# Kernel tuning notes

Hardware: AMD Instinct MI355X
Metric: run time of the kernel (lower is better)

Reference implementation:

```python
import jax, jax.numpy as jnp
from jax import lax
import numpy as np

T, B, D, N = 1024, 32, 1024, 64
INIT_D_ALPHA, INIT_ALPHA_BIAS = 0.1, 2.0

def _xavier(key, n_out, n_in):
    lim = float(np.sqrt(6.0 / (n_in + n_out)))
    return jax.random.uniform(key, (n_out, n_in), jnp.float32, -lim, lim)

def setup_inputs() -> dict:
    key = jax.random.key(0)
    k = jax.random.split(key, 5)
    return {
        "x": jax.random.normal(k[0], (T, B, D), jnp.float32),
        "S0": jnp.zeros((B, N, N), jnp.float32),
        "W_k": _xavier(k[1], N, D),
        "W_v": _xavier(k[2], N, D),
        "W_q": _xavier(k[3], N, D),
        "W_alpha": _xavier(k[4], N, D),
        "d_alpha": jnp.full((N,), INIT_D_ALPHA, jnp.float32),
        "b_alpha": jnp.full((N,), INIT_ALPHA_BIAS, jnp.float32),
    }

def reference(x, S0, W_k, W_v, W_q, W_alpha, d_alpha, b_alpha):
    # Precompute all per-step projections as batched GEMMs: [T,B,N]
    k = jnp.einsum('tbd,nd->tbn', x, W_k)
    v = jnp.einsum('tbd,nd->tbn', x, W_v)
    q = jnp.einsum('tbd,nd->tbn', x, W_q)
    ax = jnp.einsum('tbd,nd->tbn', x, W_alpha)

    def step(S, inp):
        k_t, v_t, q_t, ax_t = inp  # each [B,N]
        retrieved = jnp.einsum('bij,bj->bi', S, k_t)            # S @ k
        alpha = jax.nn.sigmoid(ax_t + d_alpha * retrieved + b_alpha)  # [B,N]
        outer = v_t[:, :, None] * k_t[:, None, :]               # outer(v,k) [B,N,N]
        S = alpha[:, :, None] * S + (1.0 - alpha)[:, :, None] * outer
        h = jnp.einsum('bij,bj->bi', S, q_t)                    # S @ q
        out = h * jax.nn.silu(h)                                # self-gated
        return S, out

    S_final, output = lax.scan(step, S0, (k, v, q, ax))
    return output, S_final
```

## Files before the change

kernel.cpp:

```cpp
#include <hip/hip_runtime.h>
#include <math.h>

#define T_STEPS 1024
#define BATCH   32
#define DIM     1024
#define NST     64
#define TBN     ((size_t)T_STEPS * BATCH * NST)

typedef __attribute__((ext_vector_type(8))) short bf16x8;
typedef __attribute__((ext_vector_type(4))) float f32x4;

#define NLOG2E (-1.44269504088896340736f)

__device__ unsigned short g_khi[TBN];
__device__ unsigned short g_klo[TBN];
__device__ unsigned short g_qhi[TBN];
__device__ unsigned short g_qlo[TBN];


__device__ __forceinline__ void gload16(const float* g, float* l)
{
    __builtin_amdgcn_global_load_lds(
        (const __attribute__((address_space(1))) unsigned int*)g,
        (__attribute__((address_space(3))) unsigned int*)l, 16, 0, 0);
}

__device__ __forceinline__ void cvt8(float4 v0, float4 v1, bf16x8& hi, bf16x8& lo)
{
    float f[8] = {v0.x, v0.y, v0.z, v0.w, v1.x, v1.y, v1.z, v1.w};
    bf16x8 h, l;
    #pragma unroll
    for (int i = 0; i < 8; i++) {
        unsigned b = __float_as_uint(f[i]);
        h[i] = (short)(b >> 16);
        l[i] = (short)(__float_as_uint(f[i] - __uint_as_float(b & 0xffff0000u)) >> 16);
    }
    hi = h; lo = l;
}

__global__ __launch_bounds__(512, 1)
void proj_gemm_v2(const float* __restrict__ x,
                  const float* __restrict__ Wk,
                  const float* __restrict__ Wv,
                  const float* __restrict__ Wq,
                  const float* __restrict__ Wa,
                  const float* __restrict__ b_alpha,
                  float* __restrict__ ws)
{
    __shared__ float As[2][128][32];
    __shared__ float Bs[2][256][32];

    const int tid  = threadIdx.x;
    const int lane = tid & 63;
    const int w    = tid >> 6;
    const int m0   = blockIdx.x * 128;

    const int lrow  = lane >> 3;
    const int lgran = (lane & 7) ^ lrow;
    const float* ap0 = x + (size_t)(m0 + 16*w +     lrow) * DIM + lgran * 4;
    const float* ap1 = x + (size_t)(m0 + 16*w + 8 + lrow) * DIM + lgran * 4;
    const float* Wsrc = (w < 2) ? Wk : (w < 4) ? Wv : (w < 6) ? Wq : Wa;
    const float* bp0 = Wsrc + (size_t)((w & 1)*32 +  0 + lrow) * DIM + lgran * 4;
    const float* bp1 = Wsrc + (size_t)((w & 1)*32 +  8 + lrow) * DIM + lgran * 4;
    const float* bp2 = Wsrc + (size_t)((w & 1)*32 + 16 + lrow) * DIM + lgran * 4;
    const float* bp3 = Wsrc + (size_t)((w & 1)*32 + 24 + lrow) * DIM + lgran * 4;

    auto stage = [&](int kb, int buf) {
        const int ko = kb * 32;
        gload16(ap0 + ko, &As[buf][16*w     ][0]);
        gload16(ap1 + ko, &As[buf][16*w +  8][0]);
        gload16(bp0 + ko, &Bs[buf][32*w     ][0]);
        gload16(bp1 + ko, &Bs[buf][32*w +  8][0]);
        gload16(bp2 + ko, &Bs[buf][32*w + 16][0]);
        gload16(bp3 + ko, &Bs[buf][32*w + 24][0]);
    };

    const int fr = lane & 15;
    const int qi = lane >> 4;
    const int sx = fr & 7;
    const int mh = w >> 2;
    const int nq = w & 3;

    f32x4 acc[4][4];
    #pragma unroll
    for (int i = 0; i < 4; i++)
        #pragma unroll
        for (int j = 0; j < 4; j++)
            acc[i][j] = (f32x4)0.0f;

    stage(0, 0);
    __syncthreads();

    #pragma unroll 1
    for (int kb = 0; kb < 32; kb++) {
        const int buf = kb & 1;
        if (kb + 1 < 32) stage(kb + 1, buf ^ 1);

        bf16x8 ah[4], al[4], bh[4], bl[4];
        #pragma unroll
        for (int mt = 0; mt < 4; mt++) {
            const float* rp = &As[buf][mh*64 + mt*16 + fr][0];
            float4 v0 = *(const float4*)(rp + (((2*qi    ) ^ sx) * 4));
            float4 v1 = *(const float4*)(rp + (((2*qi + 1) ^ sx) * 4));
            cvt8(v0, v1, ah[mt], al[mt]);
        }
        #pragma unroll
        for (int nt = 0; nt < 4; nt++) {
            const float* rp = &Bs[buf][nq*64 + nt*16 + fr][0];
            float4 v0 = *(const float4*)(rp + (((2*qi    ) ^ sx) * 4));
            float4 v1 = *(const float4*)(rp + (((2*qi + 1) ^ sx) * 4));
            cvt8(v0, v1, bh[nt], bl[nt]);
        }
        #pragma unroll
        for (int mt = 0; mt < 4; mt++)
            #pragma unroll
            for (int nt = 0; nt < 4; nt++) {
                acc[mt][nt] = __builtin_amdgcn_mfma_f32_16x16x32_bf16(ah[mt], bh[nt], acc[mt][nt], 0, 0, 0);
                acc[mt][nt] = __builtin_amdgcn_mfma_f32_16x16x32_bf16(al[mt], bh[nt], acc[mt][nt], 0, 0, 0);
                acc[mt][nt] = __builtin_amdgcn_mfma_f32_16x16x32_bf16(ah[mt], bl[nt], acc[mt][nt], 0, 0, 0);
            }

        __syncthreads();
    }

    float* outb = ws + (size_t)nq * TBN;
    const int r0 = qi * 4;
    float bav[4];
    #pragma unroll
    for (int nt = 0; nt < 4; nt++)
        bav[nt] = (nq == 3) ? b_alpha[nt*16 + fr] : 0.0f;
    const float scl = (nq == 3) ? NLOG2E : 1.0f;
    #pragma unroll
    for (int mt = 0; mt < 4; mt++)
        #pragma unroll
        for (int nt = 0; nt < 4; nt++)
            #pragma unroll
            for (int r = 0; r < 4; r++) {
                const float val = (acc[mt][nt][r] + bav[nt]) * scl;
                const size_t idx = (size_t)(m0 + mh*64 + mt*16 + r0 + r) * NST + nt*16 + fr;
                if (nq != 2)
                    outb[idx] = val;
                if (nq == 0 || nq == 2) {
                    const unsigned bits = __float_as_uint(val);
                    const unsigned short hi = (unsigned short)(bits >> 16);
                    const float lof = val - __uint_as_float(bits & 0xffff0000u);
                    const unsigned short lo = (unsigned short)(__float_as_uint(lof) >> 16);
                    if (nq == 0) { g_khi[idx] = hi; g_klo[idx] = lo; }
                    else         { g_qhi[idx] = hi; g_qlo[idx] = lo; }
                }
            }
}


#define SCH 16
#define NCH (T_STEPS / SCH)

__global__ __launch_bounds__(256, 2)
void scan_gram(const float* __restrict__ ws,
               const float* __restrict__ S0,
               const float* __restrict__ d_alpha,
               float* __restrict__ out)
{
    const float* kb_ = ws;
    const float* vb_ = ws + TBN;
    const float* ab_ = ws + 3 * TBN;

    __shared__ float k_st[2][SCH][64];
    __shared__ float va  [2][SCH][16];
    __shared__ float G_lds [SCH][16];
    __shared__ float GQ_lds[SCH][16];
    __shared__ float S_pvt[4][64];

    const int tid  = threadIdx.x;
    const int lane = tid & 63;
    const int w    = tid >> 6;
    const int bid  = blockIdx.x;
    const int b    = (bid & 7) * 4 + ((bid >> 3) & 3);
    const int rg   = bid >> 5;
    const int row  = rg * 4 + w;
    const int fr   = lane & 15;
    const int qi   = lane >> 4;

    const size_t stp = (size_t)BATCH * NST;

    float S = S0[((size_t)b * NST + row) * NST + lane];
    const float da_s = d_alpha[row] * NLOG2E;

    const float* ksrc = kb_ + (size_t)(4*w + qi) * stp + (size_t)b * NST + fr * 4;
    const float* vsrc = ((lane & 1) ? ab_ : vb_)
                      + (size_t)(lane >> 2) * stp + (size_t)b * NST + rg * 4;

    auto stage = [&](int ch, int buf) {
        gload16(ksrc + (size_t)ch * SCH * stp, &k_st[buf][4*w][0]);
        if (w == 0)
            gload16(vsrc + (size_t)ch * SCH * stp, &va[buf][0][0]);
    };

    stage(0, 0);
    __syncthreads();

    float* op = out + (size_t)b * NST + row;
    float R = 0.0f, H = 0.0f, hv = 0.0f;

    #pragma unroll 1
    for (int ch = 0; ch < NCH; ch++) {
        const int buf = ch & 1;
        if (ch + 1 < NCH) stage(ch + 1, buf ^ 1);

        const size_t fb = (size_t)ch * SCH * stp + (size_t)fr * stp + (size_t)b * NST + qi * 8;
        const bf16x8 Kh0 = *(const bf16x8*)(g_khi + fb);
        const bf16x8 Kh1 = *(const bf16x8*)(g_khi + fb + 32);
        const bf16x8 Kl0 = *(const bf16x8*)(g_klo + fb);
        const bf16x8 Kl1 = *(const bf16x8*)(g_klo + fb + 32);
        const bf16x8 Qh0 = *(const bf16x8*)(g_qhi + fb);
        const bf16x8 Qh1 = *(const bf16x8*)(g_qhi + fb + 32);
        const bf16x8 Ql0 = *(const bf16x8*)(g_qlo + fb);
        const bf16x8 Ql1 = *(const bf16x8*)(g_qlo + fb + 32);

        S_pvt[w][lane] = S;
        bf16x8 Sh0, Sl0, Sh1, Sl1;
        {
            float4 s0 = *(const float4*)&S_pvt[w][qi * 8];
            float4 s1 = *(const float4*)&S_pvt[w][qi * 8 + 4];
            cvt8(s0, s1, Sh0, Sl0);
            float4 s2 = *(const float4*)&S_pvt[w][32 + qi * 8];
            float4 s3 = *(const float4*)&S_pvt[w][32 + qi * 8 + 4];
            cvt8(s2, s3, Sh1, Sl1);
        }

        f32x4 aG = (f32x4)0.0f, aGQ = (f32x4)0.0f;
        f32x4 aR0 = (f32x4)0.0f, aR1 = (f32x4)0.0f;
        f32x4 aH0 = (f32x4)0.0f, aH1 = (f32x4)0.0f;

        aG = __builtin_amdgcn_mfma_f32_16x16x32_bf16(Kh0, Kh0, aG, 0, 0, 0);
        aG = __builtin_amdgcn_mfma_f32_16x16x32_bf16(Kh0, Kl0, aG, 0, 0, 0);
        aG = __builtin_amdgcn_mfma_f32_16x16x32_bf16(Kl0, Kh0, aG, 0, 0, 0);
        aG = __builtin_amdgcn_mfma_f32_16x16x32_bf16(Kh1, Kh1, aG, 0, 0, 0);
        aG = __builtin_amdgcn_mfma_f32_16x16x32_bf16(Kh1, Kl1, aG, 0, 0, 0);
        aG = __builtin_amdgcn_mfma_f32_16x16x32_bf16(Kl1, Kh1, aG, 0, 0, 0);

        aGQ = __builtin_amdgcn_mfma_f32_16x16x32_bf16(Kh0, Qh0, aGQ, 0, 0, 0);
        aGQ = __builtin_amdgcn_mfma_f32_16x16x32_bf16(Kh0, Ql0, aGQ, 0, 0, 0);
        aGQ = __builtin_amdgcn_mfma_f32_16x16x32_bf16(Kl0, Qh0, aGQ, 0, 0, 0);
        aGQ = __builtin_amdgcn_mfma_f32_16x16x32_bf16(Kh1, Qh1, aGQ, 0, 0, 0);
        aGQ = __builtin_amdgcn_mfma_f32_16x16x32_bf16(Kh1, Ql1, aGQ, 0, 0, 0);
        aGQ = __builtin_amdgcn_mfma_f32_16x16x32_bf16(Kl1, Qh1, aGQ, 0, 0, 0);

        aR0 = __builtin_amdgcn_mfma_f32_16x16x32_bf16(Sh0, Kh0, aR0, 0, 0, 0);
        aR0 = __builtin_amdgcn_mfma_f32_16x16x32_bf16(Sh0, Kl0, aR0, 0, 0, 0);
        aR0 = __builtin_amdgcn_mfma_f32_16x16x32_bf16(Sl0, Kh0, aR0, 0, 0, 0);
        aR1 = __builtin_amdgcn_mfma_f32_16x16x32_bf16(Sh1, Kh1, aR1, 0, 0, 0);
        aR1 = __builtin_amdgcn_mfma_f32_16x16x32_bf16(Sh1, Kl1, aR1, 0, 0, 0);
        aR1 = __builtin_amdgcn_mfma_f32_16x16x32_bf16(Sl1, Kh1, aR1, 0, 0, 0);

        aH0 = __builtin_amdgcn_mfma_f32_16x16x32_bf16(Sh0, Qh0, aH0, 0, 0, 0);
        aH0 = __builtin_amdgcn_mfma_f32_16x16x32_bf16(Sh0, Ql0, aH0, 0, 0, 0);
        aH0 = __builtin_amdgcn_mfma_f32_16x16x32_bf16(Sl0, Qh0, aH0, 0, 0, 0);
        aH1 = __builtin_amdgcn_mfma_f32_16x16x32_bf16(Sh1, Qh1, aH1, 0, 0, 0);
        aH1 = __builtin_amdgcn_mfma_f32_16x16x32_bf16(Sh1, Ql1, aH1, 0, 0, 0);
        aH1 = __builtin_amdgcn_mfma_f32_16x16x32_bf16(Sl1, Qh1, aH1, 0, 0, 0);

        #pragma unroll
        for (int r = 0; r < 4; r++) {
            G_lds [qi*4 + r][fr] = aG[r];
            GQ_lds[qi*4 + r][fr] = aGQ[r];
        }
        R = aR0[0] + aR1[0];
        H = aH0[0] + aH1[0];

        #pragma unroll
        for (int s = 0; s < SCH; s++) {
            const float kcv = k_st[buf][s][lane];
            const float Gv  = G_lds [s][fr];
            const float GQv = GQ_lds[s][fr];
            const float vv  = va[buf][s][w];
            const float aa  = va[buf][s][4 + w];

            const float ret   = __int_as_float(
                __builtin_amdgcn_readlane(__float_as_int(R), s));
            const float z     = fmaf(da_s, ret, aa);
            const float e     = __builtin_amdgcn_exp2f(z);
            const float alpha = __builtin_amdgcn_rcpf(1.0f + e);
            const float bt    = (1.0f - alpha) * vv;

            R = fmaf(alpha, R, bt * Gv);
            H = fmaf(alpha, H, bt * GQv);
            S = fmaf(alpha, S, bt * kcv);

            hv = (lane == s) ? H : hv;
        }

        {
            const float zz = hv * NLOG2E;
            const float sg = __builtin_amdgcn_rcpf(1.0f + __builtin_amdgcn_exp2f(zz));
            const float o  = hv * hv * sg;
            if (lane < SCH)
                op[(size_t)(ch * SCH + lane) * stp] = o;
        }

        __syncthreads();
    }

    out[TBN + ((size_t)b * NST + row) * NST + lane] = S;
}


extern "C" void kernel_launch(void* const* d_in, const int* in_sizes, int n_in,
                              void* d_out, int out_size, void* d_ws, size_t ws_size,
                              hipStream_t stream)
{
    const float* x  = (const float*)d_in[0];
    const float* S0 = (const float*)d_in[1];
    const float* Wk = (const float*)d_in[2];
    const float* Wv = (const float*)d_in[3];
    const float* Wq = (const float*)d_in[4];
    const float* Wa = (const float*)d_in[5];
    const float* da = (const float*)d_in[6];
    const float* ba = (const float*)d_in[7];
    float* out = (float*)d_out;
    float* ws  = (float*)d_ws;

    proj_gemm_v2<<<dim3((T_STEPS * BATCH) / 128), 512, 0, stream>>>(x, Wk, Wv, Wq, Wa, ba, ws);

    scan_gram<<<dim3(BATCH * 16), 256, 0, stream>>>(ws, S0, da, out);
}
```

Before: 436.1 us.

## Stage bf16 split K/Q planes through swizzled LDS and split Gram MFMAs across waves

K and Q hi/lo bf16 planes are now prefetched into double-buffered, XOR-swizzled LDS with global_load_lds, replacing per-chunk direct global vector loads that sat on the critical path. The Gram matrices K·K and K·Q are computed by only one wave each, written to a shared interleaved buffer and read back as float2, where before all four waves computed both redundantly. This adds a barrier in the middle of each chunk and moves the next-chunk prefetch after that barrier, so sync overhead and LDS footprint rise.

```diff
diff --git a/kernel.cpp b/kernel.cpp
--- a/kernel.cpp
+++ b/kernel.cpp
@@ -17,8 +17,7 @@
 __device__ unsigned short g_qhi[TBN];
 __device__ unsigned short g_qlo[TBN];
 
-
-__device__ __forceinline__ void gload16(const float* g, float* l)
+__device__ __forceinline__ void gload16(const void* g, void* l)
 {
     __builtin_amdgcn_global_load_lds(
         (const __attribute__((address_space(1))) unsigned int*)g,
@@ -37,6 +36,7 @@
     }
     hi = h; lo = l;
 }
+
 
 __global__ __launch_bounds__(512, 1)
 void proj_gemm_v2(const float* __restrict__ x,
@@ -156,10 +156,10 @@
 #define NCH (T_STEPS / SCH)
 
 __global__ __launch_bounds__(256, 2)
-void scan_gram(const float* __restrict__ ws,
-               const float* __restrict__ S0,
-               const float* __restrict__ d_alpha,
-               float* __restrict__ out)
+void scan_gram2(const float* __restrict__ ws,
+                const float* __restrict__ S0,
+                const float* __restrict__ d_alpha,
+                float* __restrict__ out)
 {
     const float* kb_ = ws;
     const float* vb_ = ws + TBN;
@@ -167,8 +167,11 @@
 
     __shared__ float k_st[2][SCH][64];
     __shared__ float va  [2][SCH][16];
-    __shared__ float G_lds [SCH][16];
-    __shared__ float GQ_lds[SCH][16];
+    __shared__ float GG  [2][SCH][16][2];
+    __shared__ unsigned short KH[2][SCH][64];
+    __shared__ unsigned short KL[2][SCH][64];
+    __shared__ unsigned short QH[2][SCH][64];
+    __shared__ unsigned short QL[2][SCH][64];
     __shared__ float S_pvt[4][64];
 
     const int tid  = threadIdx.x;
@@ -190,32 +193,45 @@
     const float* vsrc = ((lane & 1) ? ab_ : vb_)
                       + (size_t)(lane >> 2) * stp + (size_t)b * NST + rg * 4;
 
+    const unsigned short* pl_g = (w == 0) ? g_khi : (w == 1) ? g_klo
+                               : (w == 2) ? g_qhi : g_qlo;
+    const int prow  = lane >> 3;
+    const int pgran = (lane & 7) ^ prow;
+    const unsigned short* psrc0 = pl_g + ((size_t)prow       * stp + (size_t)b * NST + pgran * 8);
+    const unsigned short* psrc1 = pl_g + ((size_t)(8 + prow) * stp + (size_t)b * NST + pgran * 8);
+
     auto stage = [&](int ch, int buf) {
-        gload16(ksrc + (size_t)ch * SCH * stp, &k_st[buf][4*w][0]);
+        const size_t koff = (size_t)ch * SCH * stp;
+        gload16(ksrc + koff, &k_st[buf][4*w][0]);
         if (w == 0)
-            gload16(vsrc + (size_t)ch * SCH * stp, &va[buf][0][0]);
+            gload16(vsrc + koff, &va[buf][0][0]);
+        unsigned short* pdst = (w == 0) ? &KH[buf][0][0] : (w == 1) ? &KL[buf][0][0]
+                             : (w == 2) ? &QH[buf][0][0] : &QL[buf][0][0];
+        gload16(psrc0 + koff, pdst);
+        gload16(psrc1 + koff, pdst + 8 * 64);
     };
+
+    const int c1 = (qi ^ (fr & 7)) * 8;
+    const int c2 = c1 ^ 32;
 
     stage(0, 0);
     __syncthreads();
 
     float* op = out + (size_t)b * NST + row;
-    float R = 0.0f, H = 0.0f, hv = 0.0f;
+    float hv = 0.0f;
 
     #pragma unroll 1
     for (int ch = 0; ch < NCH; ch++) {
         const int buf = ch & 1;
-        if (ch + 1 < NCH) stage(ch + 1, buf ^ 1);
-
-        const size_t fb = (size_t)ch * SCH * stp + (size_t)fr * stp + (size_t)b * NST + qi * 8;
-        const bf16x8 Kh0 = *(const bf16x8*)(g_khi + fb);
-        const bf16x8 Kh1 = *(const bf16x8*)(g_khi + fb + 32);
-        const bf16x8 Kl0 = *(const bf16x8*)(g_klo + fb);
-        const bf16x8 Kl1 = *(const bf16x8*)(g_klo + fb + 32);
-        const bf16x8 Qh0 = *(const bf16x8*)(g_qhi + fb);
-        const bf16x8 Qh1 = *(const bf16x8*)(g_qhi + fb + 32);
-        const bf16x8 Ql0 = *(const bf16x8*)(g_qlo + fb);
-        const bf16x8 Ql1 = *(const bf16x8*)(g_qlo + fb + 32);
+
+        const bf16x8 Kh0 = *(const bf16x8*)&KH[buf][fr][c1];
+        const bf16x8 Kh1 = *(const bf16x8*)&KH[buf][fr][c2];
+        const bf16x8 Kl0 = *(const bf16x8*)&KL[buf][fr][c1];
+        const bf16x8 Kl1 = *(const bf16x8*)&KL[buf][fr][c2];
+        const bf16x8 Qh0 = *(const bf16x8*)&QH[buf][fr][c1];
+        const bf16x8 Qh1 = *(const bf16x8*)&QH[buf][fr][c2];
+        const bf16x8 Ql0 = *(const bf16x8*)&QL[buf][fr][c1];
+        const bf16x8 Ql1 = *(const bf16x8*)&QL[buf][fr][c2];
 
         S_pvt[w][lane] = S;
         bf16x8 Sh0, Sl0, Sh1, Sl1;
@@ -228,53 +244,55 @@
             cvt8(s2, s3, Sh1, Sl1);
         }
 
-        f32x4 aG = (f32x4)0.0f, aGQ = (f32x4)0.0f;
         f32x4 aR0 = (f32x4)0.0f, aR1 = (f32x4)0.0f;
         f32x4 aH0 = (f32x4)0.0f, aH1 = (f32x4)0.0f;
-
-        aG = __builtin_amdgcn_mfma_f32_16x16x32_bf16(Kh0, Kh0, aG, 0, 0, 0);
-        aG = __builtin_amdgcn_mfma_f32_16x16x32_bf16(Kh0, Kl0, aG, 0, 0, 0);
-        aG = __builtin_amdgcn_mfma_f32_16x16x32_bf16(Kl0, Kh0, aG, 0, 0, 0);
-        aG = __builtin_amdgcn_mfma_f32_16x16x32_bf16(Kh1, Kh1, aG, 0, 0, 0);
-        aG = __builtin_amdgcn_mfma_f32_16x16x32_bf16(Kh1, Kl1, aG, 0, 0, 0);
-        aG = __builtin_amdgcn_mfma_f32_16x16x32_bf16(Kl1, Kh1, aG, 0, 0, 0);
-
-        aGQ = __builtin_amdgcn_mfma_f32_16x16x32_bf16(Kh0, Qh0, aGQ, 0, 0, 0);
-        aGQ = __builtin_amdgcn_mfma_f32_16x16x32_bf16(Kh0, Ql0, aGQ, 0, 0, 0);
-        aGQ = __builtin_amdgcn_mfma_f32_16x16x32_bf16(Kl0, Qh0, aGQ, 0, 0, 0);
-        aGQ = __builtin_amdgcn_mfma_f32_16x16x32_bf16(Kh1, Qh1, aGQ, 0, 0, 0);
-        aGQ = __builtin_amdgcn_mfma_f32_16x16x32_bf16(Kh1, Ql1, aGQ, 0, 0, 0);
-        aGQ = __builtin_amdgcn_mfma_f32_16x16x32_bf16(Kl1, Qh1, aGQ, 0, 0, 0);
-
         aR0 = __builtin_amdgcn_mfma_f32_16x16x32_bf16(Sh0, Kh0, aR0, 0, 0, 0);
         aR0 = __builtin_amdgcn_mfma_f32_16x16x32_bf16(Sh0, Kl0, aR0, 0, 0, 0);
         aR0 = __builtin_amdgcn_mfma_f32_16x16x32_bf16(Sl0, Kh0, aR0, 0, 0, 0);
         aR1 = __builtin_amdgcn_mfma_f32_16x16x32_bf16(Sh1, Kh1, aR1, 0, 0, 0);
         aR1 = __builtin_amdgcn_mfma_f32_16x16x32_bf16(Sh1, Kl1, aR1, 0, 0, 0);
         aR1 = __builtin_amdgcn_mfma_f32_16x16x32_bf16(Sl1, Kh1, aR1, 0, 0, 0);
-
         aH0 = __builtin_amdgcn_mfma_f32_16x16x32_bf16(Sh0, Qh0, aH0, 0, 0, 0);
         aH0 = __builtin_amdgcn_mfma_f32_16x16x32_bf16(Sh0, Ql0, aH0, 0, 0, 0);
         aH0 = __builtin_amdgcn_mfma_f32_16x16x32_bf16(Sl0, Qh0, aH0, 0, 0, 0);
         aH1 = __builtin_amdgcn_mfma_f32_16x16x32_bf16(Sh1, Qh1, aH1, 0, 0, 0);
         aH1 = __builtin_amdgcn_mfma_f32_16x16x32_bf16(Sh1, Ql1, aH1, 0, 0, 0);
         aH1 = __builtin_amdgcn_mfma_f32_16x16x32_bf16(Sl1, Qh1, aH1, 0, 0, 0);
-
-        #pragma unroll
-        for (int r = 0; r < 4; r++) {
-            G_lds [qi*4 + r][fr] = aG[r];
-            GQ_lds[qi*4 + r][fr] = aGQ[r];
-        }
-        R = aR0[0] + aR1[0];
-        H = aH0[0] + aH1[0];
+        float R = aR0[0] + aR1[0];
+        float H = aH0[0] + aH1[0];
+
+        if (w == 0) {
+            f32x4 aG = (f32x4)0.0f;
+            aG = __builtin_amdgcn_mfma_f32_16x16x32_bf16(Kh0, Kh0, aG, 0, 0, 0);
+            aG = __builtin_amdgcn_mfma_f32_16x16x32_bf16(Kh0, Kl0, aG, 0, 0, 0);
+            aG = __builtin_amdgcn_mfma_f32_16x16x32_bf16(Kl0, Kh0, aG, 0, 0, 0);
+            aG = __builtin_amdgcn_mfma_f32_16x16x32_bf16(Kh1, Kh1, aG, 0, 0, 0);
+            aG = __builtin_amdgcn_mfma_f32_16x16x32_bf16(Kh1, Kl1, aG, 0, 0, 0);
+            aG = __builtin_amdgcn_mfma_f32_16x16x32_bf16(Kl1, Kh1, aG, 0, 0, 0);
+            #pragma unroll
+            for (int r = 0; r < 4; r++) GG[buf][qi*4 + r][fr][0] = aG[r];
+        } else if (w == 1) {
+            f32x4 aQ = (f32x4)0.0f;
+            aQ = __builtin_amdgcn_mfma_f32_16x16x32_bf16(Kh0, Qh0, aQ, 0, 0, 0);
+            aQ = __builtin_amdgcn_mfma_f32_16x16x32_bf16(Kh0, Ql0, aQ, 0, 0, 0);
+            aQ = __builtin_amdgcn_mfma_f32_16x16x32_bf16(Kl0, Qh0, aQ, 0, 0, 0);
+            aQ = __builtin_amdgcn_mfma_f32_16x16x32_bf16(Kh1, Qh1, aQ, 0, 0, 0);
+            aQ = __builtin_amdgcn_mfma_f32_16x16x32_bf16(Kh1, Ql1, aQ, 0, 0, 0);
+            aQ = __builtin_amdgcn_mfma_f32_16x16x32_bf16(Kl1, Qh1, aQ, 0, 0, 0);
+            #pragma unroll
+            for (int r = 0; r < 4; r++) GG[buf][qi*4 + r][fr][1] = aQ[r];
+        }
+
+        __syncthreads();
+
+        if (ch + 1 < NCH) stage(ch + 1, buf ^ 1);
 
         #pragma unroll
         for (int s = 0; s < SCH; s++) {
-            const float kcv = k_st[buf][s][lane];
-            const float Gv  = G_lds [s][fr];
-            const float GQv = GQ_lds[s][fr];
-            const float vv  = va[buf][s][w];
-            const float aa  = va[buf][s][4 + w];
+            const float  kcv = k_st[buf][s][lane];
+            const float2 g2  = *(const float2*)&GG[buf][s][fr][0];
+            const float  vv  = va[buf][s][w];
+            const float  aa  = va[buf][s][4 + w];
 
             const float ret   = __int_as_float(
                 __builtin_amdgcn_readlane(__float_as_int(R), s));
@@ -283,16 +301,15 @@
             const float alpha = __builtin_amdgcn_rcpf(1.0f + e);
             const float bt    = (1.0f - alpha) * vv;
 
-            R = fmaf(alpha, R, bt * Gv);
-            H = fmaf(alpha, H, bt * GQv);
+            R = fmaf(alpha, R, bt * g2.x);
+            H = fmaf(alpha, H, bt * g2.y);
             S = fmaf(alpha, S, bt * kcv);
 
             hv = (lane == s) ? H : hv;
         }
 
         {
-            const float zz = hv * NLOG2E;
-            const float sg = __builtin_amdgcn_rcpf(1.0f + __builtin_amdgcn_exp2f(zz));
+            const float sg = __builtin_amdgcn_rcpf(1.0f + __builtin_amdgcn_exp2f(hv * NLOG2E));
             const float o  = hv * hv * sg;
             if (lane < SCH)
                 op[(size_t)(ch * SCH + lane) * stp] = o;
@@ -322,5 +339,5 @@
 
     proj_gemm_v2<<<dim3((T_STEPS * BATCH) / 128), 512, 0, stream>>>(x, Wk, Wv, Wq, Wa, ba, ws);
 
-    scan_gram<<<dim3(BATCH * 16), 256, 0, stream>>>(ws, S0, da, out);
-}
+    scan_gram2<<<dim3(BATCH * 16), 256, 0, stream>>>(ws, S0, da, out);
+}
```

Measured after the change: 382.2 us. 12.3% less time.
